# Optimization experiments

Measured on AMD Instinct MI355X. Metric: run time of the kernel, lower is better.

Reference implementation:

```python
import jax, jax.numpy as jnp
import numpy as np

DIM = 512
HID = 512
H = 8
HD = HID // H
RB_HID = 64
COORD = 3


def setup_inputs() -> dict:
    key = jax.random.key(0)
    ks = jax.random.split(key, 12)
    B, Nq, Nk = 2, 1024, 2048
    s = 0.02
    return {
        "q_in": jax.random.normal(ks[0], (B, Nq, DIM), jnp.float32),
        "kv_in": jax.random.normal(ks[1], (B, Nk, DIM), jnp.float32),
        "q_coords": jax.random.normal(ks[2], (B, Nq, COORD), jnp.float32),
        "kv_coords": jax.random.normal(ks[3], (B, Nk, COORD), jnp.float32),
        "Wq": jax.random.normal(ks[4], (DIM, HID), jnp.float32) * s,
        "Wk": jax.random.normal(ks[5], (DIM, HID), jnp.float32) * s,
        "Wv": jax.random.normal(ks[6], (DIM, HID), jnp.float32) * s,
        "Wo": jax.random.normal(ks[7], (HID, DIM), jnp.float32) * s,
        "W1": jax.random.normal(ks[8], (1, RB_HID), jnp.float32) * s,
        "b1": jnp.zeros((RB_HID,), jnp.float32),
        "W2": jax.random.normal(ks[9], (RB_HID, H), jnp.float32) * s,
        "b2": jnp.zeros((H,), jnp.float32),
    }


def reference(q_in, kv_in, q_coords, kv_coords, Wq, Wk, Wv, Wo, W1, b1, W2, b2):
    B, Nq, _ = q_in.shape
    Nk = kv_in.shape[1]
    # projections -> [B, H, N, HD]
    q = (q_in @ Wq).reshape(B, Nq, H, HD).transpose(0, 2, 1, 3)
    k = (kv_in @ Wk).reshape(B, Nk, H, HD).transpose(0, 2, 1, 3)
    v = (kv_in @ Wv).reshape(B, Nk, H, HD).transpose(0, 2, 1, 3)
    # pairwise Euclidean distance [B, Nq, Nk]
    diff = q_coords[:, :, None, :] - kv_coords[:, None, :, :]
    d = jnp.sqrt(jnp.sum(diff * diff, axis=-1))
    # 2-layer MLP on distance -> per-head bias [B, H, Nq, Nk]
    h = jax.nn.silu(d[..., None] * W1[0] + b1)  # [B,Nq,Nk,RB_HID]
    bias = (h @ W2 + b2).transpose(0, 3, 1, 2)  # [B,H,Nq,Nk]
    scale = HD ** -0.5
    logits = jnp.einsum("bhqd,bhkd->bhqk", q, k) * scale + bias
    attn = jax.nn.softmax(logits, axis=-1)
    out = jnp.einsum("bhqk,bhkd->bhqd", attn, v)
    out = out.transpose(0, 2, 1, 3).reshape(B, Nq, HID)
    return out @ Wo
```

## Files before the change

### kernel.cpp

```cpp
#include <hip/hip_runtime.h>
#include <hip/hip_bf16.h>
#include <hip/hip_fp16.h>
#include <math.h>

typedef short bf16x8 __attribute__((ext_vector_type(8)));
typedef float f32x4 __attribute__((ext_vector_type(4)));
typedef unsigned short u16;
typedef unsigned int u32;

#define NH 8
#define BB 2
#define NQ 1024
#define NK 2048
#define M2CONST 6.4921250
#define SC2 0.18033688f

#define MFMA16(a, b, c) __builtin_amdgcn_mfma_f32_16x16x32_bf16(a, b, c, 0, 0, 0)

__device__ __constant__ double XN_D[6] = {15.727406610312546, 13.656854249492380,
                                          10.070552360820166, 5.9294476391798335,
                                          2.3431457505076194, 0.27259338968745405};
#define XN0 15.727406610312546f
#define XN1 13.656854249492380f
#define XN2 10.070552360820166f
#define XN3 5.9294476391798335f
#define XN4 2.3431457505076194f

static __device__ __forceinline__ u16 f2us(float x) {
  union { __hip_bfloat16 b; u16 u; } cv;
  cv.b = __float2bfloat16(x);
  return cv.u;
}

static __device__ __forceinline__ bf16x8 pack8(float4 a, float4 b) {
  bf16x8 r;
  r[0] = (short)f2us(a.x); r[1] = (short)f2us(a.y);
  r[2] = (short)f2us(a.z); r[3] = (short)f2us(a.w);
  r[4] = (short)f2us(b.x); r[5] = (short)f2us(b.y);
  r[6] = (short)f2us(b.z); r[7] = (short)f2us(b.w);
  return r;
}

__global__ __launch_bounds__(256) void setup_kernel(
    const float* __restrict__ Wq, const float* __restrict__ Wk,
    const float* __restrict__ Wv, const float* __restrict__ Wo,
    u16* __restrict__ Tq, u16* __restrict__ Tk,
    u16* __restrict__ Tv, u16* __restrict__ To,
    const float* __restrict__ W1, const float* __restrict__ b1,
    const float* __restrict__ W2, const float* __restrict__ b2,
    float* __restrict__ polyc,
    const float* __restrict__ kc, u16* __restrict__ keg) {
  const int blk = blockIdx.x, t = threadIdx.x;
  if (blk < 256) {
    __shared__ u16 tile[64][65];
    const float* W; u16* Wt;
    switch (blk >> 6) {
      case 0: W = Wq; Wt = Tq; break;
      case 1: W = Wk; Wt = Tk; break;
      case 2: W = Wv; Wt = Tv; break;
      default: W = Wo; Wt = To; break;
    }
    const int rem = blk & 63;
    const int k0 = (rem >> 3) * 64, n0 = (rem & 7) * 64;
    const int r = t >> 4, c4 = (t & 15) * 4;
    #pragma unroll
    for (int p = 0; p < 4; p++) {
      int row = p * 16 + r;
      float4 v = *(const float4*)&W[(size_t)(k0 + row) * 512 + n0 + c4];
      tile[row][c4 + 0] = f2us(v.x);
      tile[row][c4 + 1] = f2us(v.y);
      tile[row][c4 + 2] = f2us(v.z);
      tile[row][c4 + 3] = f2us(v.w);
    }
    __syncthreads();
    #pragma unroll
    for (int p = 0; p < 4; p++) {
      int n = p * 16 + r;
      u16 u0 = tile[c4 + 0][n], u1 = tile[c4 + 1][n];
      u16 u2 = tile[c4 + 2][n], u3 = tile[c4 + 3][n];
      uint2 o;
      o.x = u0 | ((u32)u1 << 16);
      o.y = u2 | ((u32)u3 << 16);
      *(uint2*)&Wt[(size_t)(n0 + n) * 512 + k0 + c4] = o;
    }
  } else if (blk == 256) {
    __shared__ double fv[6][8];
    if (t < 48) {
      int i = t >> 3, h = t & 7;
      double x = XN_D[i];
      double acc = (double)b2[h];
      for (int r = 0; r < 64; r++) {
        double u = x * (double)W1[r] + (double)b1[r];
        double s = u / (1.0 + exp(-u));
        acc += s * (double)W2[r * 8 + h];
      }
      fv[i][h] = acc * 1.4426950408889634 - M2CONST;
    }
    __syncthreads();
    if (t < 8) {
      int h = t;
      double c[6];
      #pragma unroll
      for (int i = 0; i < 6; i++) c[i] = fv[i][h];
      for (int k = 1; k < 6; k++)
        for (int i = 5; i >= k; i--)
          c[i] = (c[i] - c[i - 1]) / (XN_D[i] - XN_D[i - k]);
      #pragma unroll
      for (int j = 0; j < 6; j++) polyc[h * 8 + j] = (float)c[j];
    }
  } else {
    int r = (blk - 257) * 256 + t;
    float kx = kc[(size_t)r * 3], ky = kc[(size_t)r * 3 + 1], kz = kc[(size_t)r * 3 + 2];
    uint4 o;
    o.x = f2us(-2.0f * kx) | ((u32)f2us(-2.0f * ky) << 16);
    o.y = f2us(-2.0f * kz) | ((u32)f2us(1.0f) << 16);
    o.z = (u32)f2us(kx * kx + ky * ky + kz * kz);
    o.w = 0;
    *(uint4*)&keg[(size_t)r * 8] = o;
  }
}

__global__ __launch_bounds__(256) void gemm_qkv(
    const float* __restrict__ q_in, const float* __restrict__ kv_in,
    const u16* __restrict__ Wqt, const u16* __restrict__ Wkt,
    const u16* __restrict__ Wvt, u16* __restrict__ Qp,
    u16* __restrict__ Kp, u16* __restrict__ Vtp) {
  __shared__ u16 As[64 * 72];
  __shared__ u16 Bs[64 * 72];
  __shared__ u16 Bs2[64 * 72];
  const int t = threadIdx.x;
  const int w = t >> 6, l = t & 63, g = l >> 4, li = l & 15;
  const int bx = blockIdx.x;
  const bool isQ = bx < 32;
  const int m0 = (isQ ? bx : bx - 32) * 64, n0 = blockIdx.y * 64;
  const float* A = isQ ? q_in : kv_in;
  const u16* B1 = isQ ? Wqt : Wkt;
  const int ms = (w & 1) * 32, ns = (w >> 1) * 32;
  const int ar = t >> 2, ac = (t & 3) * 16;
  f32x4 acc[2][2] = {}, accV[2][2] = {};

  for (int kt = 0; kt < 512; kt += 64) {
    float4 a4[4];
    #pragma unroll
    for (int q = 0; q < 4; q++)
      a4[q] = *(const float4*)&A[(size_t)(m0 + ar) * 512 + kt + ac + 4 * q];
    bf16x8 bk[2], bv2[2];
    #pragma unroll
    for (int p = 0; p < 2; p++) {
      int f = p * 256 + t, r = f >> 3, c8 = (f & 7) * 8;
      bk[p] = *(const bf16x8*)&B1[(size_t)(n0 + r) * 512 + kt + c8];
    }
    if (!isQ) {
      #pragma unroll
      for (int p = 0; p < 2; p++) {
        int f = p * 256 + t, r = f >> 3, c8 = (f & 7) * 8;
        bv2[p] = *(const bf16x8*)&Wvt[(size_t)(n0 + r) * 512 + kt + c8];
      }
    }
    __syncthreads();
    *(bf16x8*)&As[ar * 72 + ac] = pack8(a4[0], a4[1]);
    *(bf16x8*)&As[ar * 72 + ac + 8] = pack8(a4[2], a4[3]);
    #pragma unroll
    for (int p = 0; p < 2; p++) {
      int f = p * 256 + t, r = f >> 3, c8 = (f & 7) * 8;
      *(bf16x8*)&Bs[r * 72 + c8] = bk[p];
    }
    if (!isQ) {
      #pragma unroll
      for (int p = 0; p < 2; p++) {
        int f = p * 256 + t, r = f >> 3, c8 = (f & 7) * 8;
        *(bf16x8*)&Bs2[r * 72 + c8] = bv2[p];
      }
    }
    __syncthreads();
    #pragma unroll
    for (int ks = 0; ks < 2; ks++) {
      bf16x8 a0 = *(const bf16x8*)&As[(ms + li) * 72 + ks * 32 + g * 8];
      bf16x8 a1 = *(const bf16x8*)&As[(ms + 16 + li) * 72 + ks * 32 + g * 8];
      bf16x8 k0 = *(const bf16x8*)&Bs[(ns + li) * 72 + ks * 32 + g * 8];
      bf16x8 k1 = *(const bf16x8*)&Bs[(ns + 16 + li) * 72 + ks * 32 + g * 8];
      acc[0][0] = MFMA16(a0, k0, acc[0][0]);
      acc[0][1] = MFMA16(a0, k1, acc[0][1]);
      acc[1][0] = MFMA16(a1, k0, acc[1][0]);
      acc[1][1] = MFMA16(a1, k1, acc[1][1]);
      if (!isQ) {
        bf16x8 v0 = *(const bf16x8*)&Bs2[(ns + li) * 72 + ks * 32 + g * 8];
        bf16x8 v1 = *(const bf16x8*)&Bs2[(ns + 16 + li) * 72 + ks * 32 + g * 8];
        accV[0][0] = MFMA16(a0, v0, accV[0][0]);
        accV[0][1] = MFMA16(a0, v1, accV[0][1]);
        accV[1][0] = MFMA16(a1, v0, accV[1][0]);
        accV[1][1] = MFMA16(a1, v1, accV[1][1]);
      }
    }
  }
  #pragma unroll
  for (int mi = 0; mi < 2; mi++) {
    #pragma unroll
    for (int ni = 0; ni < 2; ni++) {
      int row = m0 + ms + mi * 16 + 4 * g;
      int col = n0 + ns + ni * 16 + li;
      f32x4 vk = acc[mi][ni];
      if (isQ) {
        #pragma unroll
        for (int r = 0; r < 4; r++) Qp[(size_t)(row + r) * 512 + col] = f2us(vk[r]);
      } else {
        #pragma unroll
        for (int r = 0; r < 4; r++) Kp[(size_t)(row + r) * 512 + col] = f2us(vk[r]);
        f32x4 vv = accV[mi][ni];
        int bb = row >> 11, j = row & 2047;
        int hh = col >> 6, d = col & 63;
        uint2 o;
        o.x = f2us(vv[0]) | ((u32)f2us(vv[1]) << 16);
        o.y = f2us(vv[2]) | ((u32)f2us(vv[3]) << 16);
        *(uint2*)&Vtp[((size_t)((bb * 8 + hh) * 64 + d)) * 2048 + j] = o;
      }
    }
  }
}

__global__ __launch_bounds__(256) void gemm_wo(const u16* __restrict__ A,
                                               const u16* __restrict__ Bt,
                                               float* __restrict__ C) {
  __shared__ u16 As[32 * 72];
  __shared__ u16 Bs[64 * 72];
  const int t = threadIdx.x;
  const int w = t >> 6, l = t & 63, g = l >> 4, li = l & 15;
  const int m0 = blockIdx.x * 32, n0 = blockIdx.y * 64;
  const int ms = (w & 1) * 16, ns = (w >> 1) * 32;
  f32x4 acc[2] = {};
  for (int kt = 0; kt < 512; kt += 64) {
    bf16x8 av, bv[2];
    {
      int r = t >> 3, c8 = (t & 7) * 8;
      av = *(const bf16x8*)&A[(size_t)(m0 + r) * 512 + kt + c8];
    }
    #pragma unroll
    for (int p = 0; p < 2; p++) {
      int f = p * 256 + t, r = f >> 3, c8 = (f & 7) * 8;
      bv[p] = *(const bf16x8*)&Bt[(size_t)(n0 + r) * 512 + kt + c8];
    }
    __syncthreads();
    {
      int r = t >> 3, c8 = (t & 7) * 8;
      *(bf16x8*)&As[r * 72 + c8] = av;
    }
    #pragma unroll
    for (int p = 0; p < 2; p++) {
      int f = p * 256 + t, r = f >> 3, c8 = (f & 7) * 8;
      *(bf16x8*)&Bs[r * 72 + c8] = bv[p];
    }
    __syncthreads();
    #pragma unroll
    for (int ks = 0; ks < 2; ks++) {
      bf16x8 af = *(const bf16x8*)&As[(ms + li) * 72 + ks * 32 + g * 8];
      bf16x8 b0 = *(const bf16x8*)&Bs[(ns + li) * 72 + ks * 32 + g * 8];
      bf16x8 b1 = *(const bf16x8*)&Bs[(ns + 16 + li) * 72 + ks * 32 + g * 8];
      acc[0] = MFMA16(af, b0, acc[0]);
      acc[1] = MFMA16(af, b1, acc[1]);
    }
  }
  #pragma unroll
  for (int ni = 0; ni < 2; ni++) {
    f32x4 v = acc[ni];
    int row = m0 + ms + 4 * g;
    int col = n0 + ns + ni * 16 + li;
    #pragma unroll
    for (int r = 0; r < 4; r++) C[(size_t)(row + r) * 512 + col] = v[r];
  }
}

__global__ __launch_bounds__(256, 4) void attn_kernel(
    const u16* __restrict__ Qb, const u16* __restrict__ Kb,
    const u16* __restrict__ Vt, const float* __restrict__ qc,
    const u16* __restrict__ keg, const float* __restrict__ polyc,
    float* __restrict__ Op, float* __restrict__ Lp) {
  __shared__ u16 Kl[64 * 72];
  __shared__ u16 Vtl[64 * 72];
  __shared__ u16 Pl[64 * 72];

  const int t = threadIdx.x;
  const int w = t >> 6, l = t & 63, g = l >> 4, li = l & 15;
  const int qt = blockIdx.x >> 2, sidx = blockIdx.x & 3;
  const int h = blockIdx.y, b = blockIdx.z;

  const float c0 = polyc[h * 8 + 0], c1 = polyc[h * 8 + 1];
  const float c2 = polyc[h * 8 + 2], c3 = polyc[h * 8 + 3];
  const float c4 = polyc[h * 8 + 4], c5 = polyc[h * 8 + 5];

  const int qrow = qt * 64 + w * 16 + li;
  const size_t qg = (size_t)b * NQ + qrow;
  bf16x8 qf0 = *(const bf16x8*)&Qb[qg * 512 + h * 64 + g * 8];
  bf16x8 qf1 = *(const bf16x8*)&Qb[qg * 512 + h * 64 + 32 + g * 8];
  float qx = qc[qg * 3], qy = qc[qg * 3 + 1], qz = qc[qg * 3 + 2];
  bf16x8 qe = {};
  if (g == 0) {
    qe[0] = (short)f2us(qx);
    qe[1] = (short)f2us(qy);
    qe[2] = (short)f2us(qz);
    qe[3] = (short)f2us(qx * qx + qy * qy + qz * qz);
    qe[4] = (short)f2us(1.0f);
  }

  f32x4 oacc[4] = {};
  float lacc = 0.0f;

  const u16* Kg = Kb + (size_t)b * NK * 512 + h * 64;
  const u16* Vg = Vt + (size_t)((b * 8 + h) * 64) * 2048;
  const u16* keg_b = keg + (size_t)b * NK * 8;

  for (int it = 0; it < 8; it++) {
    const int jbase = sidx * 512 + it * 64;
    __syncthreads();
    #pragma unroll
    for (int pp = 0; pp < 2; pp++) {
      int f = pp * 256 + t, row = f >> 3, c8 = (f & 7) * 8;
      *(bf16x8*)&Kl[row * 72 + c8] =
          *(const bf16x8*)&Kg[(size_t)(jbase + row) * 512 + c8];
      *(bf16x8*)&Vtl[row * 72 + c8] =
          *(const bf16x8*)&Vg[(size_t)row * 2048 + jbase + c8];
    }
    __syncthreads();

    f32x4 sac[4], dac[4];
    #pragma unroll
    for (int j4 = 0; j4 < 4; j4++) {
      bf16x8 ka0 = *(const bf16x8*)&Kl[(j4 * 16 + li) * 72 + g * 8];
      bf16x8 ka1 = *(const bf16x8*)&Kl[(j4 * 16 + li) * 72 + 32 + g * 8];
      f32x4 z = {};
      f32x4 s0 = MFMA16(ka0, qf0, z);
      sac[j4] = MFMA16(ka1, qf1, s0);
      bf16x8 ke = {};
      if (g == 0)
        ke = *(const bf16x8*)&keg_b[(size_t)(jbase + j4 * 16 + li) * 8];
      dac[j4] = MFMA16(ke, qe, z);
    }

    #pragma unroll
    for (int j4 = 0; j4 < 4; j4++) {
      float p[4];
      #pragma unroll
      for (int r = 0; r < 4; r++) {
        float u = fmaxf(dac[j4][r], 0.0f);
        float d = fminf(sqrtf(u), 16.0f);
        float gp = c5;
        gp = fmaf(gp, d - XN4, c4);
        gp = fmaf(gp, d - XN3, c3);
        gp = fmaf(gp, d - XN2, c2);
        gp = fmaf(gp, d - XN1, c1);
        gp = fmaf(gp, d - XN0, c0);
        p[r] = exp2f(fmaf(sac[j4][r], SC2, gp));
        lacc += p[r];
      }
      uint2 pv;
      pv.x = f2us(p[0]) | ((u32)f2us(p[1]) << 16);
      pv.y = f2us(p[2]) | ((u32)f2us(p[3]) << 16);
      *(uint2*)&Pl[(w * 16 + li) * 72 + j4 * 16 + g * 4] = pv;
    }

    bf16x8 pf0 = *(const bf16x8*)&Pl[(w * 16 + li) * 72 + g * 8];
    bf16x8 pf1 = *(const bf16x8*)&Pl[(w * 16 + li) * 72 + 32 + g * 8];
    #pragma unroll
    for (int dt = 0; dt < 4; dt++) {
      bf16x8 v0 = *(const bf16x8*)&Vtl[(dt * 16 + li) * 72 + g * 8];
      bf16x8 v1 = *(const bf16x8*)&Vtl[(dt * 16 + li) * 72 + 32 + g * 8];
      oacc[dt] = MFMA16(pf0, v0, oacc[dt]);
      oacc[dt] = MFMA16(pf1, v1, oacc[dt]);
    }
  }

  float lf = lacc;
  lf += __shfl_xor(lf, 16);
  lf += __shfl_xor(lf, 32);

  const size_t obase =
      ((size_t)(sidx * 16 + b * 8 + h) * 1024 + qt * 64 + w * 16) * 64;
  #pragma unroll
  for (int dt = 0; dt < 4; dt++)
    #pragma unroll
    for (int r = 0; r < 4; r++)
      Op[obase + (size_t)(4 * g + r) * 64 + dt * 16 + li] = oacc[dt][r];
  if (g == 0)
    Lp[(size_t)(sidx * 16 + b * 8 + h) * 1024 + qt * 64 + w * 16 + li] = lf;
}

__global__ __launch_bounds__(256) void combine_kernel(const float* __restrict__ Op,
                                                      const float* __restrict__ Lp,
                                                      u16* __restrict__ AOb) {
  int tid = blockIdx.x * 256 + threadIdx.x;
  int d4 = tid & 15, rh = tid >> 4;
  int bh = rh >> 10, qrow = rh & 1023;
  f32x4 o = {};
  float lsum = 0.0f;
  #pragma unroll
  for (int s = 0; s < 4; s++) {
    f32x4 v = *(const f32x4*)&Op[((size_t)(s * 16 + bh) * 1024 + qrow) * 64 + d4 * 4];
    o += v;
    lsum += Lp[(size_t)(s * 16 + bh) * 1024 + qrow];
  }
  float inv = 1.0f / lsum;
  uint2 pk;
  pk.x = f2us(o[0] * inv) | ((u32)f2us(o[1] * inv) << 16);
  pk.y = f2us(o[2] * inv) | ((u32)f2us(o[3] * inv) << 16);
  *(uint2*)&AOb[((size_t)(bh >> 3) * NQ + qrow) * 512 + (bh & 7) * 64 + d4 * 4] = pk;
}

extern "C" void kernel_launch(void* const* d_in, const int* in_sizes, int n_in,
                              void* d_out, int out_size, void* d_ws, size_t ws_size,
                              hipStream_t stream) {
  const float* q_in      = (const float*)d_in[0];
  const float* kv_in     = (const float*)d_in[1];
  const float* q_coords  = (const float*)d_in[2];
  const float* kv_coords = (const float*)d_in[3];
  const float* Wq        = (const float*)d_in[4];
  const float* Wk        = (const float*)d_in[5];
  const float* Wv        = (const float*)d_in[6];
  const float* Wo        = (const float*)d_in[7];
  const float* W1        = (const float*)d_in[8];
  const float* b1        = (const float*)d_in[9];
  const float* W2        = (const float*)d_in[10];
  const float* b2        = (const float*)d_in[11];

  char* p = (char*)d_ws;
  u16* Wqt  = (u16*)p; p += (size_t)512 * 512 * 2;
  u16* Wkt  = (u16*)p; p += (size_t)512 * 512 * 2;
  u16* Wvt  = (u16*)p; p += (size_t)512 * 512 * 2;
  u16* Wot  = (u16*)p; p += (size_t)512 * 512 * 2;
  u16* Qp   = (u16*)p; p += (size_t)2048 * 512 * 2;
  u16* Kp   = (u16*)p; p += (size_t)4096 * 512 * 2;
  u16* Vtp  = (u16*)p; p += (size_t)4096 * 512 * 2;
  u16* AOb  = (u16*)p; p += (size_t)2048 * 512 * 2;
  u16* keg  = (u16*)p; p += (size_t)4096 * 8 * 2;
  float* polyc = (float*)p; p += (size_t)64 * 4;
  p = (char*)(((size_t)p + 255) & ~(size_t)255);
  float* Opart = (float*)p; p += (size_t)4 * 16 * 1024 * 64 * 4;
  float* Lpart = (float*)p; p += (size_t)4 * 16 * 1024 * 4;

  setup_kernel<<<273, 256, 0, stream>>>(Wq, Wk, Wv, Wo, Wqt, Wkt, Wvt, Wot,
                                        W1, b1, W2, b2, polyc, kv_coords, keg);
  gemm_qkv<<<dim3(96, 8), 256, 0, stream>>>(q_in, kv_in, Wqt, Wkt, Wvt,
                                            Qp, Kp, Vtp);
  attn_kernel<<<dim3(64, 8, 2), 256, 0, stream>>>(Qp, Kp, Vtp, q_coords, keg,
                                                  polyc, Opart, Lpart);
  combine_kernel<<<1024, 256, 0, stream>>>(Opart, Lpart, AOb);
  gemm_wo<<<dim3(64, 8), 256, 0, stream>>>(AOb, Wot, (float*)d_out);
}
```

Baseline: 158.2 us.

## Fuse split-K combine into output projection GEMM and use fast intrinsics

```diff
diff --git a/kernel.cpp b/kernel.cpp
--- a/kernel.cpp
+++ b/kernel.cpp
@@ -1,6 +1,5 @@
 #include <hip/hip_runtime.h>
 #include <hip/hip_bf16.h>
-#include <hip/hip_fp16.h>
 #include <math.h>
 
 typedef short bf16x8 __attribute__((ext_vector_type(8)));
@@ -32,13 +31,22 @@
   return cv.u;
 }
 
+static __device__ __forceinline__ u32 bfr(float x) {
+  u32 u = __builtin_bit_cast(u32, x);
+  return u + 0x7FFFu + ((u >> 16) & 1u);
+}
+static __device__ __forceinline__ u32 pk2(float lo, float hi) {
+  return (bfr(lo) >> 16) | (bfr(hi) & 0xFFFF0000u);
+}
+static __device__ __forceinline__ u16 bfs(float x) { return (u16)(bfr(x) >> 16); }
+
 static __device__ __forceinline__ bf16x8 pack8(float4 a, float4 b) {
-  bf16x8 r;
-  r[0] = (short)f2us(a.x); r[1] = (short)f2us(a.y);
-  r[2] = (short)f2us(a.z); r[3] = (short)f2us(a.w);
-  r[4] = (short)f2us(b.x); r[5] = (short)f2us(b.y);
-  r[6] = (short)f2us(b.z); r[7] = (short)f2us(b.w);
-  return r;
+  union { bf16x8 v; uint4 u; } cv;
+  cv.u.x = pk2(a.x, a.y);
+  cv.u.y = pk2(a.z, a.w);
+  cv.u.z = pk2(b.x, b.y);
+  cv.u.w = pk2(b.z, b.w);
+  return cv.v;
 }
 
 __global__ __launch_bounds__(256) void setup_kernel(
@@ -202,70 +210,19 @@
       f32x4 vk = acc[mi][ni];
       if (isQ) {
         #pragma unroll
-        for (int r = 0; r < 4; r++) Qp[(size_t)(row + r) * 512 + col] = f2us(vk[r]);
+        for (int r = 0; r < 4; r++) Qp[(size_t)(row + r) * 512 + col] = bfs(vk[r]);
       } else {
         #pragma unroll
-        for (int r = 0; r < 4; r++) Kp[(size_t)(row + r) * 512 + col] = f2us(vk[r]);
+        for (int r = 0; r < 4; r++) Kp[(size_t)(row + r) * 512 + col] = bfs(vk[r]);
         f32x4 vv = accV[mi][ni];
         int bb = row >> 11, j = row & 2047;
         int hh = col >> 6, d = col & 63;
         uint2 o;
-        o.x = f2us(vv[0]) | ((u32)f2us(vv[1]) << 16);
-        o.y = f2us(vv[2]) | ((u32)f2us(vv[3]) << 16);
+        o.x = pk2(vv[0], vv[1]);
+        o.y = pk2(vv[2], vv[3]);
         *(uint2*)&Vtp[((size_t)((bb * 8 + hh) * 64 + d)) * 2048 + j] = o;
       }
     }
-  }
-}
-
-__global__ __launch_bounds__(256) void gemm_wo(const u16* __restrict__ A,
-                                               const u16* __restrict__ Bt,
-                                               float* __restrict__ C) {
-  __shared__ u16 As[32 * 72];
-  __shared__ u16 Bs[64 * 72];
-  const int t = threadIdx.x;
-  const int w = t >> 6, l = t & 63, g = l >> 4, li = l & 15;
-  const int m0 = blockIdx.x * 32, n0 = blockIdx.y * 64;
-  const int ms = (w & 1) * 16, ns = (w >> 1) * 32;
-  f32x4 acc[2] = {};
-  for (int kt = 0; kt < 512; kt += 64) {
-    bf16x8 av, bv[2];
-    {
-      int r = t >> 3, c8 = (t & 7) * 8;
-      av = *(const bf16x8*)&A[(size_t)(m0 + r) * 512 + kt + c8];
-    }
-    #pragma unroll
-    for (int p = 0; p < 2; p++) {
-      int f = p * 256 + t, r = f >> 3, c8 = (f & 7) * 8;
-      bv[p] = *(const bf16x8*)&Bt[(size_t)(n0 + r) * 512 + kt + c8];
-    }
-    __syncthreads();
-    {
-      int r = t >> 3, c8 = (t & 7) * 8;
-      *(bf16x8*)&As[r * 72 + c8] = av;
-    }
-    #pragma unroll
-    for (int p = 0; p < 2; p++) {
-      int f = p * 256 + t, r = f >> 3, c8 = (f & 7) * 8;
-      *(bf16x8*)&Bs[r * 72 + c8] = bv[p];
-    }
-    __syncthreads();
-    #pragma unroll
-    for (int ks = 0; ks < 2; ks++) {
-      bf16x8 af = *(const bf16x8*)&As[(ms + li) * 72 + ks * 32 + g * 8];
-      bf16x8 b0 = *(const bf16x8*)&Bs[(ns + li) * 72 + ks * 32 + g * 8];
-      bf16x8 b1 = *(const bf16x8*)&Bs[(ns + 16 + li) * 72 + ks * 32 + g * 8];
-      acc[0] = MFMA16(af, b0, acc[0]);
-      acc[1] = MFMA16(af, b1, acc[1]);
-    }
-  }
-  #pragma unroll
-  for (int ni = 0; ni < 2; ni++) {
-    f32x4 v = acc[ni];
-    int row = m0 + ms + 4 * g;
-    int col = n0 + ns + ni * 16 + li;
-    #pragma unroll
-    for (int r = 0; r < 4; r++) C[(size_t)(row + r) * 512 + col] = v[r];
   }
 }
 
@@ -341,19 +298,19 @@
       #pragma unroll
       for (int r = 0; r < 4; r++) {
         float u = fmaxf(dac[j4][r], 0.0f);
-        float d = fminf(sqrtf(u), 16.0f);
+        float d = fminf(__builtin_amdgcn_sqrtf(u), 16.0f);
         float gp = c5;
         gp = fmaf(gp, d - XN4, c4);
         gp = fmaf(gp, d - XN3, c3);
         gp = fmaf(gp, d - XN2, c2);
         gp = fmaf(gp, d - XN1, c1);
         gp = fmaf(gp, d - XN0, c0);
-        p[r] = exp2f(fmaf(sac[j4][r], SC2, gp));
+        p[r] = __builtin_amdgcn_exp2f(fmaf(sac[j4][r], SC2, gp));
         lacc += p[r];
       }
       uint2 pv;
-      pv.x = f2us(p[0]) | ((u32)f2us(p[1]) << 16);
-      pv.y = f2us(p[2]) | ((u32)f2us(p[3]) << 16);
+      pv.x = pk2(p[0], p[1]);
+      pv.y = pk2(p[2], p[3]);
       *(uint2*)&Pl[(w * 16 + li) * 72 + j4 * 16 + g * 4] = pv;
     }
 
@@ -383,25 +340,71 @@
     Lp[(size_t)(sidx * 16 + b * 8 + h) * 1024 + qt * 64 + w * 16 + li] = lf;
 }
 
-__global__ __launch_bounds__(256) void combine_kernel(const float* __restrict__ Op,
-                                                      const float* __restrict__ Lp,
-                                                      u16* __restrict__ AOb) {
-  int tid = blockIdx.x * 256 + threadIdx.x;
-  int d4 = tid & 15, rh = tid >> 4;
-  int bh = rh >> 10, qrow = rh & 1023;
-  f32x4 o = {};
-  float lsum = 0.0f;
+__global__ __launch_bounds__(256) void gemm_wo(const float* __restrict__ Op,
+                                               const float* __restrict__ Lp,
+                                               const u16* __restrict__ Bt,
+                                               float* __restrict__ C) {
+  __shared__ u16 As[32 * 72];
+  __shared__ u16 Bs[64 * 72];
+  const int t = threadIdx.x;
+  const int w = t >> 6, l = t & 63, g = l >> 4, li = l & 15;
+  const int m0 = blockIdx.x * 32, n0 = blockIdx.y * 64;
+  const int ms = (w & 1) * 16, ns = (w >> 1) * 32;
+  const int arow = t >> 3, ac8 = (t & 7) * 8;
+  const int bq = (m0 + arow) >> 10, qrow = (m0 + arow) & 1023;
+  f32x4 acc[2] = {};
+
+  for (int kt = 0; kt < 512; kt += 64) {
+    const int h = kt >> 6;
+    const int bh = bq * 8 + h;
+    f32x4 s0 = {}, s1 = {};
+    float lsum = 0.0f;
+    #pragma unroll
+    for (int s = 0; s < 4; s++) {
+      const float* base = &Op[((size_t)(s * 16 + bh) * 1024 + qrow) * 64 + ac8];
+      s0 += *(const f32x4*)base;
+      s1 += *(const f32x4*)(base + 4);
+      lsum += Lp[(size_t)(s * 16 + bh) * 1024 + qrow];
+    }
+    float inv = __builtin_amdgcn_rcpf(lsum);
+    bf16x8 bv[2];
+    #pragma unroll
+    for (int p = 0; p < 2; p++) {
+      int f = p * 256 + t, r = f >> 3, c8 = (f & 7) * 8;
+      bv[p] = *(const bf16x8*)&Bt[(size_t)(n0 + r) * 512 + kt + c8];
+    }
+    __syncthreads();
+    {
+      union { bf16x8 v; uint4 u; } cv;
+      cv.u.x = pk2(s0[0] * inv, s0[1] * inv);
+      cv.u.y = pk2(s0[2] * inv, s0[3] * inv);
+      cv.u.z = pk2(s1[0] * inv, s1[1] * inv);
+      cv.u.w = pk2(s1[2] * inv, s1[3] * inv);
+      *(bf16x8*)&As[arow * 72 + ac8] = cv.v;
+    }
+    #pragma unroll
+    for (int p = 0; p < 2; p++) {
+      int f = p * 256 + t, r = f >> 3, c8 = (f & 7) * 8;
+      *(bf16x8*)&Bs[r * 72 + c8] = bv[p];
+    }
+    __syncthreads();
+    #pragma unroll
+    for (int ks = 0; ks < 2; ks++) {
+      bf16x8 af = *(const bf16x8*)&As[(ms + li) * 72 + ks * 32 + g * 8];
+      bf16x8 b0 = *(const bf16x8*)&Bs[(ns + li) * 72 + ks * 32 + g * 8];
+      bf16x8 b1 = *(const bf16x8*)&Bs[(ns + 16 + li) * 72 + ks * 32 + g * 8];
+      acc[0] = MFMA16(af, b0, acc[0]);
+      acc[1] = MFMA16(af, b1, acc[1]);
+    }
+  }
   #pragma unroll
-  for (int s = 0; s < 4; s++) {
-    f32x4 v = *(const f32x4*)&Op[((size_t)(s * 16 + bh) * 1024 + qrow) * 64 + d4 * 4];
-    o += v;
-    lsum += Lp[(size_t)(s * 16 + bh) * 1024 + qrow];
-  }
-  float inv = 1.0f / lsum;
-  uint2 pk;
-  pk.x = f2us(o[0] * inv) | ((u32)f2us(o[1] * inv) << 16);
-  pk.y = f2us(o[2] * inv) | ((u32)f2us(o[3] * inv) << 16);
-  *(uint2*)&AOb[((size_t)(bh >> 3) * NQ + qrow) * 512 + (bh & 7) * 64 + d4 * 4] = pk;
+  for (int ni = 0; ni < 2; ni++) {
+    f32x4 v = acc[ni];
+    int row = m0 + ms + 4 * g;
+    int col = n0 + ns + ni * 16 + li;
+    #pragma unroll
+    for (int r = 0; r < 4; r++) C[(size_t)(row + r) * 512 + col] = v[r];
+  }
 }
 
 extern "C" void kernel_launch(void* const* d_in, const int* in_sizes, int n_in,
@@ -428,7 +431,6 @@
   u16* Qp   = (u16*)p; p += (size_t)2048 * 512 * 2;
   u16* Kp   = (u16*)p; p += (size_t)4096 * 512 * 2;
   u16* Vtp  = (u16*)p; p += (size_t)4096 * 512 * 2;
-  u16* AOb  = (u16*)p; p += (size_t)2048 * 512 * 2;
   u16* keg  = (u16*)p; p += (size_t)4096 * 8 * 2;
   float* polyc = (float*)p; p += (size_t)64 * 4;
   p = (char*)(((size_t)p + 255) & ~(size_t)255);
@@ -441,6 +443,5 @@
                                             Qp, Kp, Vtp);
   attn_kernel<<<dim3(64, 8, 2), 256, 0, stream>>>(Qp, Kp, Vtp, q_coords, keg,
                                                   polyc, Opart, Lpart);
-  combine_kernel<<<1024, 256, 0, stream>>>(Opart, Lpart, AOb);
-  gemm_wo<<<dim3(64, 8), 256, 0, stream>>>(AOb, Wot, (float*)d_out);
-}
+  gemm_wo<<<dim3(64, 8), 256, 0, stream>>>(Opart, Lpart, Wot, (float*)d_out);
+}
```

Measured after the change: 152.7 us. -3.5%, faster.
